# Performance work log

Hardware: AMD Instinct MI355X
Metric: run time of the kernel (lower is better)

The kernel has to match this reference:

```python
import jax, jax.numpy as jnp
import numpy as np

N_SYNAPSES = 2097152  # 2**21 synapse weights in the object graph
PATH_LEN = 16         # length of each dynamic_wander path


def setup_inputs() -> dict:
    key = jax.random.key(0)
    k1, k2, k3 = jax.random.split(key, 3)
    x = jax.random.normal(k1, (2048, 2048), dtype=jnp.float32)
    n = x.size
    # Precomputed wander paths: synapse indices visited per input scalar.
    paths = jax.random.randint(k2, (n, PATH_LEN), 0, N_SYNAPSES, dtype=jnp.int64)
    # Synapse weights near 1.0 so a 16-step product stays well-conditioned.
    weights = (jnp.float32(1.0) + 0.05 * jax.random.normal(k3, (N_SYNAPSES,), dtype=jnp.float32))
    return {"x": x, "paths": paths, "weights": weights}


def reference(x, paths, weights):
    # Gather synapse weights along each element's wander path: [N, L]
    w_path = weights[paths]
    # Value propagates multiplicatively through the path's synapses.
    out_flat = x.reshape(-1) * jnp.prod(w_path, axis=1)
    return out_flat.reshape(x.shape)
```

## Files before the change

kernel.cpp:

```cpp
#include <hip/hip_runtime.h>

typedef int v4i __attribute__((ext_vector_type(4)));

#define LOG2_CHUNK 19
#define NCHUNK 4

__global__ __launch_bounds__(256) void marble_wander_kernel(
    const float* __restrict__ x,
    const int*   __restrict__ paths,
    const float* __restrict__ weights,
    float*       __restrict__ out,
    int n)
{
    int i = blockIdx.x * blockDim.x + threadIdx.x;
    bool valid = (i < n);
    int ii = valid ? i : 0;

    const v4i* p = reinterpret_cast<const v4i*>(paths) + (size_t)ii * 4;
    v4i p0 = __builtin_nontemporal_load(p + 0);
    v4i p1 = __builtin_nontemporal_load(p + 1);
    v4i p2 = __builtin_nontemporal_load(p + 2);
    v4i p3 = __builtin_nontemporal_load(p + 3);

    int idx[16] = { p0.x, p0.y, p0.z, p0.w,
                    p1.x, p1.y, p1.z, p1.w,
                    p2.x, p2.y, p2.z, p2.w,
                    p3.x, p3.y, p3.z, p3.w };

    float a0 = 1.0f, a1 = 1.0f, a2 = 1.0f, a3 = 1.0f;

    #pragma unroll
    for (int c = 0; c < NCHUNK; ++c) {
        #pragma unroll
        for (int j = 0; j < 16; ++j) {
            if ((((unsigned)idx[j]) >> LOG2_CHUNK) == (unsigned)c) {
                float w = weights[idx[j]];
                if      ((j & 3) == 0) a0 *= w;
                else if ((j & 3) == 1) a1 *= w;
                else if ((j & 3) == 2) a2 *= w;
                else                   a3 *= w;
            }
        }
        __syncthreads();
    }

    float xv = __builtin_nontemporal_load(&x[ii]);
    float r  = xv * ((a0 * a1) * (a2 * a3));
    if (valid) __builtin_nontemporal_store(r, &out[i]);
}

extern "C" void kernel_launch(void* const* d_in, const int* in_sizes, int n_in,
                              void* d_out, int out_size, void* d_ws, size_t ws_size,
                              hipStream_t stream) {
    const float* x       = (const float*)d_in[0];
    const int*   paths   = (const int*)d_in[1];
    const float* weights = (const float*)d_in[2];
    float*       out     = (float*)d_out;

    int n = in_sizes[0];
    int block = 256;
    int grid = (n + block - 1) / block;
    marble_wander_kernel<<<grid, block, 0, stream>>>(x, paths, weights, out, n);
}
```

Before: 669.2 us.

## Sort path indices per thread instead of chunked gather passes with barriers

Replaces the four chunk-filtered gather passes, each ending in a block barrier, with a 16-element sorting network on each thread's path indices followed by a single unconditional gather and a tree product. Each thread then issues its gathers in ascending address order, without the per-chunk branches and barriers. This gives up the block-wide chunk synchronization that kept lanes gathering from the same 2MB region at the same time, which may hurt L2 locality. It also adds about 60 min/max operations per thread.

```diff
diff --git a/kernel.cpp b/kernel.cpp
--- a/kernel.cpp
+++ b/kernel.cpp
@@ -1,9 +1,6 @@
 #include <hip/hip_runtime.h>
 
 typedef int v4i __attribute__((ext_vector_type(4)));
-
-#define LOG2_CHUNK 19
-#define NCHUNK 4
 
 __global__ __launch_bounds__(256) void marble_wander_kernel(
     const float* __restrict__ x,
@@ -22,30 +19,46 @@
     v4i p2 = __builtin_nontemporal_load(p + 2);
     v4i p3 = __builtin_nontemporal_load(p + 3);
 
-    int idx[16] = { p0.x, p0.y, p0.z, p0.w,
-                    p1.x, p1.y, p1.z, p1.w,
-                    p2.x, p2.y, p2.z, p2.w,
-                    p3.x, p3.y, p3.z, p3.w };
+    unsigned idx[16] = { (unsigned)p0.x, (unsigned)p0.y, (unsigned)p0.z, (unsigned)p0.w,
+                         (unsigned)p1.x, (unsigned)p1.y, (unsigned)p1.z, (unsigned)p1.w,
+                         (unsigned)p2.x, (unsigned)p2.y, (unsigned)p2.z, (unsigned)p2.w,
+                         (unsigned)p3.x, (unsigned)p3.y, (unsigned)p3.z, (unsigned)p3.w };
 
-    float a0 = 1.0f, a1 = 1.0f, a2 = 1.0f, a3 = 1.0f;
+    #define CE(a,b) { unsigned lo_ = min(idx[a], idx[b]); \
+                      unsigned hi_ = max(idx[a], idx[b]); \
+                      idx[a] = lo_; idx[b] = hi_; }
+    CE(0,1)  CE(2,3)  CE(4,5)  CE(6,7)  CE(8,9)  CE(10,11) CE(12,13) CE(14,15)
+    CE(0,2)  CE(1,3)  CE(4,6)  CE(5,7)  CE(8,10) CE(9,11)  CE(12,14) CE(13,15)
+    CE(1,2)  CE(5,6)  CE(9,10) CE(13,14)
+    CE(0,4)  CE(1,5)  CE(2,6)  CE(3,7)  CE(8,12) CE(9,13)  CE(10,14) CE(11,15)
+    CE(2,4)  CE(3,5)  CE(10,12) CE(11,13)
+    CE(1,2)  CE(3,4)  CE(5,6)  CE(9,10) CE(11,12) CE(13,14)
+    CE(0,8)  CE(1,9)  CE(2,10) CE(3,11) CE(4,12) CE(5,13)  CE(6,14)  CE(7,15)
+    CE(4,8)  CE(5,9)  CE(6,10) CE(7,11)
+    CE(2,4)  CE(3,5)  CE(6,8)  CE(7,9)  CE(10,12) CE(11,13)
+    CE(1,2)  CE(3,4)  CE(5,6)  CE(7,8)  CE(9,10) CE(11,12) CE(13,14)
+    #undef CE
 
+    float w[16];
     #pragma unroll
-    for (int c = 0; c < NCHUNK; ++c) {
-        #pragma unroll
-        for (int j = 0; j < 16; ++j) {
-            if ((((unsigned)idx[j]) >> LOG2_CHUNK) == (unsigned)c) {
-                float w = weights[idx[j]];
-                if      ((j & 3) == 0) a0 *= w;
-                else if ((j & 3) == 1) a1 *= w;
-                else if ((j & 3) == 2) a2 *= w;
-                else                   a3 *= w;
-            }
-        }
-        __syncthreads();
-    }
+    for (int j = 0; j < 16; ++j) w[j] = weights[idx[j]];
+
+    float a0 = w[0]  * w[1];
+    float a1 = w[2]  * w[3];
+    float a2 = w[4]  * w[5];
+    float a3 = w[6]  * w[7];
+    float a4 = w[8]  * w[9];
+    float a5 = w[10] * w[11];
+    float a6 = w[12] * w[13];
+    float a7 = w[14] * w[15];
+    float b0 = a0 * a1;
+    float b1 = a2 * a3;
+    float b2 = a4 * a5;
+    float b3 = a6 * a7;
+    float prod = (b0 * b1) * (b2 * b3);
 
     float xv = __builtin_nontemporal_load(&x[ii]);
-    float r  = xv * ((a0 * a1) * (a2 * a3));
+    float r  = xv * prod;
     if (valid) __builtin_nontemporal_store(r, &out[i]);
 }
 
```

Measured after the change: 860.6 us. 1.29x slower.

## Gather from fp16 copy of synapse weights instead of chunked fp32 phases

Applied to the files above, without the earlier changes.

Adds a pre-pass that converts the fp32 weight table into a half-precision copy in workspace. The main kernel then gathers all 16 path weights directly from this smaller table and multiplies them in fp32 in a tree, with no chunked synchronised phases. This halves the footprint of the randomly accessed table so more of it can stay cached. In exchange the weights are rounded to fp16, which adds relative error to the product, and an extra conversion kernel runs each call. The old phased kernel remains as a fallback when the workspace is too small.

```diff
diff --git a/kernel.cpp b/kernel.cpp
--- a/kernel.cpp
+++ b/kernel.cpp
@@ -1,11 +1,70 @@
 #include <hip/hip_runtime.h>
+#include <hip/hip_fp16.h>
 
 typedef int v4i __attribute__((ext_vector_type(4)));
 
+#define N_SYNAPSES (1 << 21)
+
+__global__ __launch_bounds__(256) void convert_weights_f16(
+    const float* __restrict__ weights,
+    __half*      __restrict__ wh)
+{
+    int i = blockIdx.x * blockDim.x + threadIdx.x;
+    float4 w = reinterpret_cast<const float4*>(weights)[i];
+    __half2 h0 = __floats2half2_rn(w.x, w.y);
+    __half2 h1 = __floats2half2_rn(w.z, w.w);
+    reinterpret_cast<__half2*>(wh)[2 * i + 0] = h0;
+    reinterpret_cast<__half2*>(wh)[2 * i + 1] = h1;
+}
+
+__global__ __launch_bounds__(256) void marble_gather_f16(
+    const float*  __restrict__ x,
+    const int*    __restrict__ paths,
+    const __half* __restrict__ wh,
+    float*        __restrict__ out,
+    int n)
+{
+    int i = blockIdx.x * blockDim.x + threadIdx.x;
+    bool valid = (i < n);
+    int ii = valid ? i : 0;
+
+    const v4i* p = reinterpret_cast<const v4i*>(paths) + (size_t)ii * 4;
+    v4i p0 = __builtin_nontemporal_load(p + 0);
+    v4i p1 = __builtin_nontemporal_load(p + 1);
+    v4i p2 = __builtin_nontemporal_load(p + 2);
+    v4i p3 = __builtin_nontemporal_load(p + 3);
+
+    int idx[16] = { p0.x, p0.y, p0.z, p0.w,
+                    p1.x, p1.y, p1.z, p1.w,
+                    p2.x, p2.y, p2.z, p2.w,
+                    p3.x, p3.y, p3.z, p3.w };
+
+    __half w[16];
+    #pragma unroll
+    for (int j = 0; j < 16; ++j) w[j] = wh[idx[j]];
+
+    float f[16];
+    #pragma unroll
+    for (int j = 0; j < 16; ++j) f[j] = __half2float(w[j]);
+
+    float a0 = f[0]  * f[1];
+    float a1 = f[2]  * f[3];
+    float a2 = f[4]  * f[5];
+    float a3 = f[6]  * f[7];
+    float a4 = f[8]  * f[9];
+    float a5 = f[10] * f[11];
+    float a6 = f[12] * f[13];
+    float a7 = f[14] * f[15];
+    float prod = ((a0 * a1) * (a2 * a3)) * ((a4 * a5) * (a6 * a7));
+
+    float xv = __builtin_nontemporal_load(&x[ii]);
+    float r  = xv * prod;
+    if (valid) __builtin_nontemporal_store(r, &out[i]);
+}
+
 #define LOG2_CHUNK 19
 #define NCHUNK 4
-
-__global__ __launch_bounds__(256) void marble_wander_kernel(
+__global__ __launch_bounds__(256) void marble_wander_phased(
     const float* __restrict__ x,
     const int*   __restrict__ paths,
     const float* __restrict__ weights,
@@ -28,7 +87,6 @@
                     p3.x, p3.y, p3.z, p3.w };
 
     float a0 = 1.0f, a1 = 1.0f, a2 = 1.0f, a3 = 1.0f;
-
     #pragma unroll
     for (int c = 0; c < NCHUNK; ++c) {
         #pragma unroll
@@ -60,5 +118,12 @@
     int n = in_sizes[0];
     int block = 256;
     int grid = (n + block - 1) / block;
-    marble_wander_kernel<<<grid, block, 0, stream>>>(x, paths, weights, out, n);
+
+    if (ws_size >= (size_t)N_SYNAPSES * sizeof(__half)) {
+        __half* wh = (__half*)d_ws;
+        convert_weights_f16<<<N_SYNAPSES / 4 / 256, 256, 0, stream>>>(weights, wh);
+        marble_gather_f16<<<grid, block, 0, stream>>>(x, paths, wh, out, n);
+    } else {
+        marble_wander_phased<<<grid, block, 0, stream>>>(x, paths, weights, out, n);
+    }
 }
```

New measurement: 656.5 us. About the same (-1.9%).
